# Kernel optimization log

Measured on AMD Instinct MI355X. Metric: run time of the kernel, lower is better.

The kernel has to match this reference:

```python
import jax, jax.numpy as jnp
import numpy as np

H, D, R, S, K, EV = 8, 256, 6, 2, 2, 2   # num_heads, head_dim, ratio, shared_head, topk, expand_v
HID = 2048
DV = D * EV            # head_v_dim = 512
KEY_DIM = H * D        # 2048
VAL_DIM = KEY_DIM * EV # 4096


def setup_inputs() -> dict:
    key = jax.random.key(0)
    ks = jax.random.split(key, 9)
    b, t = 2, 1024
    def lin(k, fan_in, shape):
        # ~torch default linear init scale
        return jax.random.normal(k, shape, jnp.float32) * (fan_in ** -0.5)
    return {
        "hidden_states": jax.random.normal(ks[0], (b, t, HID), jnp.float32),
        "Wq": lin(ks[1], HID, (HID, KEY_DIM)),
        "Wk": lin(ks[2], HID, (HID, KEY_DIM)),
        "Wv": lin(ks[3], HID, (HID, VAL_DIM)),
        "Wq_exp": lin(ks[4], D, (H, D, D * R)),  # per-head q expert expansion (ModuleList -> batched)
        "Wk_exp": lin(ks[5], D, (H, D, D * R)),
        "Wgate": lin(ks[6], D, (D, R - S)),
        "Wg": lin(ks[7], HID, (HID, VAL_DIM)),
        "Wo": lin(ks[8], VAL_DIM, (VAL_DIM, HID)),
    }


def reference(hidden_states, Wq, Wk, Wv, Wq_exp, Wk_exp, Wgate, Wg, Wo):
    b, t, _ = hidden_states.shape
    # base projections, split into heads: [H, b, t, D]
    q = (hidden_states @ Wq).reshape(b, t, H, D).transpose(2, 0, 1, 3)
    k = (hidden_states @ Wk).reshape(b, t, H, D).transpose(2, 0, 1, 3)
    v = (hidden_states @ Wv).reshape(b, t, H, DV)  # [b, t, H, DV]

    # --- sparse routing on q (gate over ratio - shared experts) ---
    logits = jnp.einsum('hbtd,dn->hbtn', q, Wgate)
    scores = jax.nn.softmax(logits.astype(jnp.float32), axis=-1)
    w, idx = jax.lax.top_k(scores, K)
    w = w / jnp.sum(w, axis=-1, keepdims=True)
    idx = idx + S  # shift past shared experts
    # scatter top-k weights into full [H, b, t, R]
    full = jnp.sum(jax.nn.one_hot(idx, R, dtype=w.dtype) * w[..., None], axis=-2)
    full = full.at[..., :S].set(1.0 / S)
    full = full / jnp.sum(full, axis=-1, keepdims=True)
    rw = full.astype(hidden_states.dtype).transpose(3, 1, 2, 0)  # [R, b, t, H]
    mask = (rw != 0).astype(hidden_states.dtype)                 # [R, b, t, H]

    # --- per-head expert expansions: [R, b, t, H, D] ---
    qe = jnp.einsum('hbtd,hde->hbte', q, Wq_exp).reshape(H, b, t, R, D).transpose(3, 1, 2, 0, 4)
    ke = jnp.einsum('hbtd,hde->hbte', k, Wk_exp).reshape(H, b, t, R, D).transpose(3, 1, 2, 0, 4)
    ve = jnp.broadcast_to(v[None], (R, b, t, H, DV))
    qe = qe * mask[..., None]
    ke = ke * mask[..., None]
    ve = ve * mask[..., None]

    # --- dense attention per (expert, batch, head) ---
    attn = jax.nn.softmax(jnp.einsum('rbqhd,rbkhd->rbhqk', qe, ke) / (D ** 0.5), axis=-1)
    o = jnp.einsum('rbhqk,rbkhd->rbqhd', attn, ve)  # [R, b, t, H, DV]

    # --- weighted combine over experts + gated output ---
    o = jnp.einsum('rbthd,rbth->bthd', o, rw)
    g = (hidden_states @ Wg).reshape(b, t, H, DV)
    o = o * jax.nn.silu(g)
    return o.reshape(b, t, VAL_DIM) @ Wo
```

## Files before the change

kernel.cpp:

```cpp
#include <hip/hip_runtime.h>
#include <hip/hip_bf16.h>
#include <cstdint>
#include <cstddef>

typedef __bf16 bf16_t;
typedef __bf16 bf16x8 __attribute__((ext_vector_type(8)));
typedef float f32x4 __attribute__((ext_vector_type(4)));

typedef __attribute__((address_space(3))) unsigned int lds_uint_t;
typedef __attribute__((address_space(1))) unsigned int glob_uint_t;

__device__ __forceinline__ void gload16(const void* g, void* l) {
  __builtin_amdgcn_global_load_lds((const glob_uint_t*)g, (lds_uint_t*)l, 16, 0, 0);
}

__device__ __forceinline__ f32x4 mfma16(bf16x8 a, bf16x8 b, f32x4 c) {
  return __builtin_amdgcn_mfma_f32_16x16x32_bf16(a, b, c, 0, 0, 0);
}

__global__ __launch_bounds__(256) void conv_bf16_k(const float* __restrict__ in,
                                                   bf16_t* __restrict__ out, int n8) {
  int i = blockIdx.x * 256 + threadIdx.x;
  if (i >= n8) return;
  f32x4 a = *(const f32x4*)(in + (size_t)i * 8);
  f32x4 b = *(const f32x4*)(in + (size_t)i * 8 + 4);
  bf16x8 o;
  o[0] = (bf16_t)a[0]; o[1] = (bf16_t)a[1]; o[2] = (bf16_t)a[2]; o[3] = (bf16_t)a[3];
  o[4] = (bf16_t)b[0]; o[5] = (bf16_t)b[1]; o[6] = (bf16_t)b[2]; o[7] = (bf16_t)b[3];
  *(bf16x8*)(out + (size_t)i * 8) = o;
}

__global__ __launch_bounds__(256) void tconv_k(const float* __restrict__ in, bf16_t* __restrict__ out,
                                               int R, int C, size_t inZ, size_t outZ) {
  __shared__ __align__(16) bf16_t t[64 * 72];
  in += (size_t)blockIdx.z * inZ;
  out += (size_t)blockIdx.z * outZ;
  const int c0 = blockIdx.x * 64, r0 = blockIdx.y * 64;
  const int tid = threadIdx.x;
#pragma unroll
  for (int it = 0; it < 4; it++) {
    int c = tid + it * 256;
    int row = c >> 4, ch = c & 15;
    f32x4 v = *(const f32x4*)(in + (size_t)(r0 + row) * C + c0 + ch * 4);
#pragma unroll
    for (int j = 0; j < 4; j++) t[(ch * 4 + j) * 72 + row] = (bf16_t)v[j];
  }
  __syncthreads();
#pragma unroll
  for (int it = 0; it < 2; it++) {
    int c = tid + it * 256;
    int oc = c >> 3, ch = c & 7;
    bf16x8 v = *(const bf16x8*)(t + oc * 72 + ch * 8);
    *(bf16x8*)(out + (size_t)(c0 + oc) * R + r0 + ch * 8) = v;
  }
}

__global__ __launch_bounds__(256) void tv_k(const bf16_t* __restrict__ v, bf16_t* __restrict__ Vt) {
  __shared__ __align__(16) bf16_t t[64 * 72];
  const int tt0 = blockIdx.x * 64;
  const int dv0 = blockIdx.y * 64;
  const int bh = blockIdx.z;
  const int b = bh >> 3, h = bh & 7;
  const int tid = threadIdx.x;
  const bf16_t* src = v + (size_t)(b * 1024 + tt0) * 12288 + 8192 + h * 512 + dv0;
#pragma unroll
  for (int it = 0; it < 2; it++) {
    int c = tid + it * 256;
    int row = c >> 3, ch = c & 7;
    bf16x8 x = *(const bf16x8*)(src + (size_t)row * 12288 + ch * 8);
#pragma unroll
    for (int j = 0; j < 8; j++) t[(ch * 8 + j) * 72 + row] = x[j];
  }
  __syncthreads();
  bf16_t* dst = Vt + (size_t)bh * 524288 + (size_t)dv0 * 1024 + tt0;
#pragma unroll
  for (int it = 0; it < 2; it++) {
    int c = tid + it * 256;
    int od = c >> 3, ch = c & 7;
    bf16x8 x = *(const bf16x8*)(t + od * 72 + ch * 8);
    *(bf16x8*)(dst + (size_t)od * 1024 + ch * 8) = x;
  }
}

__global__ __launch_bounds__(256) void wfuse_k(const float* __restrict__ Wq, const float* __restrict__ Wgate,
                                               float* __restrict__ Wf) {
  __shared__ float wg[1024];
  const int tid = threadIdx.x;
  for (int i = tid; i < 1024; i += 256) wg[i] = Wgate[i];
  __syncthreads();
  const int kk = blockIdx.x * 64 + (tid & 63);
  const int oid = tid >> 6;
  float acc[8] = {0, 0, 0, 0, 0, 0, 0, 0};
  const float* wr = Wq + (size_t)kk * 2048;
#pragma unroll
  for (int half = 0; half < 2; half++) {
    const int h = oid * 2 + half;
    const float* seg = wr + h * 256;
    for (int d = 0; d < 256; d += 4) {
      f32x4 q4 = *(const f32x4*)(seg + d);
#pragma unroll
      for (int n = 0; n < 4; n++) {
        acc[half * 4 + n] += q4[0] * wg[(d + 0) * 4 + n] + q4[1] * wg[(d + 1) * 4 + n] +
                             q4[2] * wg[(d + 2) * 4 + n] + q4[3] * wg[(d + 3) * 4 + n];
      }
    }
  }
#pragma unroll
  for (int jj = 0; jj < 8; jj++) Wf[(size_t)kk * 32 + oid * 8 + jj] = acc[jj];
}

__global__ __launch_bounds__(256) void logits_k(const float* __restrict__ hs, const float* __restrict__ Wf,
                                                float* __restrict__ lg) {
  __shared__ __align__(16) float hrow[2048];
  __shared__ float red[8][32];
  const int bt = blockIdx.x;
  const int tid = threadIdx.x;
  const float* src = hs + (size_t)bt * 2048;
  for (int i = tid; i < 512; i += 256) *(f32x4*)&hrow[i * 4] = *(const f32x4*)(src + i * 4);
  __syncthreads();
  const int j = tid & 31, part = tid >> 5;
  float acc = 0.f;
  for (int kk = part * 256; kk < part * 256 + 256; kk++) acc += hrow[kk] * Wf[(size_t)kk * 32 + j];
  red[part][j] = acc;
  __syncthreads();
  if (tid < 32) {
    float s = 0.f;
#pragma unroll
    for (int p = 0; p < 8; p++) s += red[p][tid];
    lg[(size_t)bt * 32 + tid] = s;
  }
}

__global__ __launch_bounds__(256) void routing_k(const float* __restrict__ lg, float* __restrict__ rw) {
  int gid = blockIdx.x * 256 + threadIdx.x;
  if (gid >= 16384) return;
  const int h = gid >> 11;
  const int bt = gid & 2047;
  const int b = bt >> 10, tt = bt & 1023;
  f32x4 l = *(const f32x4*)(lg + (size_t)bt * 32 + h * 4);
  float mx = fmaxf(fmaxf(l[0], l[1]), fmaxf(l[2], l[3]));
  float e0 = __expf(l[0] - mx), e1 = __expf(l[1] - mx), e2 = __expf(l[2] - mx), e3 = __expf(l[3] - mx);
  float den = e0 + e1 + e2 + e3;
  float s[4] = {e0 / den, e1 / den, e2 / den, e3 / den};
  int i1 = 0;
#pragma unroll
  for (int i = 1; i < 4; i++) if (s[i] > s[i1]) i1 = i;
  int i2 = (i1 == 0) ? 1 : 0;
#pragma unroll
  for (int i = 0; i < 4; i++) if (i != i1 && s[i] > s[i2]) i2 = i;
  float sw = s[i1] + s[i2];
  float w1 = s[i1] / sw, w2 = s[i2] / sw;
  float tot = 1.0f + w1 + w2;
  float o[6] = {0.5f / tot, 0.5f / tot, 0.f, 0.f, 0.f, 0.f};
  o[2 + i1] = w1 / tot;
  o[2 + i2] = w2 / tot;
#pragma unroll
  for (int r = 0; r < 6; r++) rw[(size_t)((r * 2 + b) * 8 + h) * 1024 + tt] = o[r];
}

template <int MODE>
__global__ __launch_bounds__(256) void gemm_bt(const bf16_t* __restrict__ A, const bf16_t* __restrict__ B,
                                               void* __restrict__ Cp, int K, int lda, int ldb, int ldc) {
  __shared__ __align__(16) bf16_t lsA[128 * 64];
  __shared__ __align__(16) bf16_t lsB[128 * 64];
  const int tid = threadIdx.x;
  const int lane = tid & 63, wv = tid >> 6;
  const int lrow = lane & 15, lgrp = lane >> 4;
  const int wr = wv >> 1, wc = wv & 1;
  const int bn = blockIdx.x * 128, bm = blockIdx.y * 128;

  f32x4 zero = {0.f, 0.f, 0.f, 0.f};
  f32x4 acc[4][4];
#pragma unroll
  for (int i = 0; i < 4; i++)
#pragma unroll
    for (int j = 0; j < 4; j++) acc[i][j] = zero;

  for (int k0 = 0; k0 < K; k0 += 64) {
    __syncthreads();
#pragma unroll
    for (int it = 0; it < 4; it++) {
      int c = tid + it * 256;
      int row = c >> 3, coff = (c & 7) * 16;
      gload16((const char*)A + ((size_t)(bm + row) * lda + k0) * 2 + coff, (char*)lsA + row * 128 + coff);
      gload16((const char*)B + ((size_t)(bn + row) * ldb + k0) * 2 + coff, (char*)lsB + row * 128 + coff);
    }
    __syncthreads();
#pragma unroll
    for (int kk = 0; kk < 2; kk++) {
      bf16x8 af[4], bfr[4];
#pragma unroll
      for (int m4 = 0; m4 < 4; m4++)
        af[m4] = *(const bf16x8*)((const char*)lsA + (wr * 64 + m4 * 16 + lrow) * 128 + kk * 64 + lgrp * 16);
#pragma unroll
      for (int n4 = 0; n4 < 4; n4++)
        bfr[n4] = *(const bf16x8*)((const char*)lsB + (wc * 64 + n4 * 16 + lrow) * 128 + kk * 64 + lgrp * 16);
#pragma unroll
      for (int m4 = 0; m4 < 4; m4++)
#pragma unroll
        for (int n4 = 0; n4 < 4; n4++) acc[m4][n4] = mfma16(af[m4], bfr[n4], acc[m4][n4]);
    }
  }
#pragma unroll
  for (int m4 = 0; m4 < 4; m4++) {
#pragma unroll
    for (int i = 0; i < 4; i++) {
      const int row = bm + wr * 64 + m4 * 16 + lgrp * 4 + i;
#pragma unroll
      for (int n4 = 0; n4 < 4; n4++) {
        const int col = bn + wc * 64 + n4 * 16 + lrow;
        float v = acc[m4][n4][i];
        if constexpr (MODE == 0) {
          ((bf16_t*)Cp)[(size_t)row * ldc + col] = (bf16_t)v;
        } else {
          ((float*)Cp)[(size_t)row * ldc + col] = v;
        }
      }
    }
  }
}

__global__ __launch_bounds__(256) void gemm_n64(const bf16_t* __restrict__ A, const bf16_t* __restrict__ B,
                                                float* __restrict__ C, int K, int lda, int ldb, int ldc) {
  __shared__ __align__(16) bf16_t lsA[128 * 64];
  __shared__ __align__(16) bf16_t lsB[64 * 64];
  const int tid = threadIdx.x;
  const int lane = tid & 63, wr = tid >> 6;
  const int lrow = lane & 15, lgrp = lane >> 4;
  const int bn = blockIdx.x * 64, bm = blockIdx.y * 128;

  f32x4 zero = {0.f, 0.f, 0.f, 0.f};
  f32x4 acc[2][4];
#pragma unroll
  for (int i = 0; i < 2; i++)
#pragma unroll
    for (int j = 0; j < 4; j++) acc[i][j] = zero;

  for (int k0 = 0; k0 < K; k0 += 64) {
    __syncthreads();
#pragma unroll
    for (int it = 0; it < 4; it++) {
      int c = tid + it * 256;
      int row = c >> 3, coff = (c & 7) * 16;
      gload16((const char*)A + ((size_t)(bm + row) * lda + k0) * 2 + coff, (char*)lsA + row * 128 + coff);
    }
#pragma unroll
    for (int it = 0; it < 2; it++) {
      int c = tid + it * 256;
      int row = c >> 3, coff = (c & 7) * 16;
      gload16((const char*)B + ((size_t)(bn + row) * ldb + k0) * 2 + coff, (char*)lsB + row * 128 + coff);
    }
    __syncthreads();
#pragma unroll
    for (int kk = 0; kk < 2; kk++) {
      bf16x8 af[2], bfr[4];
#pragma unroll
      for (int m2 = 0; m2 < 2; m2++)
        af[m2] = *(const bf16x8*)((const char*)lsA + (wr * 32 + m2 * 16 + lrow) * 128 + kk * 64 + lgrp * 16);
#pragma unroll
      for (int n4 = 0; n4 < 4; n4++)
        bfr[n4] = *(const bf16x8*)((const char*)lsB + (n4 * 16 + lrow) * 128 + kk * 64 + lgrp * 16);
#pragma unroll
      for (int m2 = 0; m2 < 2; m2++)
#pragma unroll
        for (int n4 = 0; n4 < 4; n4++) acc[m2][n4] = mfma16(af[m2], bfr[n4], acc[m2][n4]);
    }
  }
#pragma unroll
  for (int m2 = 0; m2 < 2; m2++) {
#pragma unroll
    for (int i = 0; i < 4; i++) {
      const int row = bm + wr * 32 + m2 * 16 + lgrp * 4 + i;
#pragma unroll
      for (int n4 = 0; n4 < 4; n4++) {
        C[(size_t)row * ldc + bn + n4 * 16 + lrow] = acc[m2][n4][i];
      }
    }
  }
}

__global__ __launch_bounds__(256) void gemm_exp(const bf16_t* __restrict__ qkg, const bf16_t* __restrict__ Wqe,
                                                const bf16_t* __restrict__ Wke, bf16_t* __restrict__ qeB,
                                                bf16_t* __restrict__ keB) {
  __shared__ __align__(16) bf16_t lsA[128 * 64];
  __shared__ __align__(16) bf16_t lsB[128 * 64];
  const int tid = threadIdx.x;
  const int lane = tid & 63, wv = tid >> 6;
  const int lrow = lane & 15, lgrp = lane >> 4;
  const int wr = wv >> 1, wc = wv & 1;
  const int bn = blockIdx.x * 128, bm = blockIdx.y * 128;
  const int z = blockIdx.z;
  const int sel = z >> 3, hh = z & 7;
  const bf16_t* A = qkg + sel * 2048 + hh * 256;
  const bf16_t* B = (sel ? Wke : Wqe) + (size_t)hh * 393216;
  bf16_t* C = sel ? keB : qeB;

  f32x4 zero = {0.f, 0.f, 0.f, 0.f};
  f32x4 acc[4][4];
#pragma unroll
  for (int i = 0; i < 4; i++)
#pragma unroll
    for (int j = 0; j < 4; j++) acc[i][j] = zero;

  for (int k0 = 0; k0 < 256; k0 += 64) {
    __syncthreads();
#pragma unroll
    for (int it = 0; it < 4; it++) {
      int c = tid + it * 256;
      int row = c >> 3, coff = (c & 7) * 16;
      gload16((const char*)A + ((size_t)(bm + row) * 12288 + k0) * 2 + coff, (char*)lsA + row * 128 + coff);
      gload16((const char*)B + ((size_t)(bn + row) * 256 + k0) * 2 + coff, (char*)lsB + row * 128 + coff);
    }
    __syncthreads();
#pragma unroll
    for (int kk = 0; kk < 2; kk++) {
      bf16x8 af[4], bfr[4];
#pragma unroll
      for (int m4 = 0; m4 < 4; m4++)
        af[m4] = *(const bf16x8*)((const char*)lsA + (wr * 64 + m4 * 16 + lrow) * 128 + kk * 64 + lgrp * 16);
#pragma unroll
      for (int n4 = 0; n4 < 4; n4++)
        bfr[n4] = *(const bf16x8*)((const char*)lsB + (wc * 64 + n4 * 16 + lrow) * 128 + kk * 64 + lgrp * 16);
#pragma unroll
      for (int m4 = 0; m4 < 4; m4++)
#pragma unroll
        for (int n4 = 0; n4 < 4; n4++) acc[m4][n4] = mfma16(af[m4], bfr[n4], acc[m4][n4]);
    }
  }
#pragma unroll
  for (int m4 = 0; m4 < 4; m4++) {
#pragma unroll
    for (int i = 0; i < 4; i++) {
      const int row = bm + wr * 64 + m4 * 16 + lgrp * 4 + i;
      const int bb = row >> 10, tt = row & 1023;
#pragma unroll
      for (int n4 = 0; n4 < 4; n4++) {
        const int col = bn + wc * 64 + n4 * 16 + lrow;
        const int rr = col >> 8, dd = col & 255;
        C[((size_t)((rr * 2 + bb) * 8 + hh) * 1024 + tt) * 256 + dd] = (bf16_t)acc[m4][n4][i];
      }
    }
  }
}

__global__ __launch_bounds__(256, 2) void attn_k(const bf16_t* __restrict__ qe, const bf16_t* __restrict__ ke,
                                                 const bf16_t* __restrict__ Vt, const float* __restrict__ rw,
                                                 const bf16_t* __restrict__ g, bf16_t* __restrict__ oc) {
  __shared__ __align__(16) bf16_t ldsK[2][32 * 256];
  __shared__ __align__(16) bf16_t ldsV[2][256 * 32];
  __shared__ __align__(16) bf16_t ldsP[4 * 16 * 40];

  const int f = (blockIdx.x & 7) * 64 + (blockIdx.x >> 3);
  const int qt = f & 15, dvh = (f >> 4) & 1, bh = f >> 5;

  const int tid = threadIdx.x;
  const int wv = tid >> 6, lane = tid & 63;
  const int lrow = lane & 15, lgrp = lane >> 4;
  const int b = bh >> 3, h = bh & 7;
  const int qw = qt * 64 + wv * 16;

  const char* vbase = (const char*)Vt + ((size_t)bh * 524288 + (size_t)dvh * 262144) * 2;

  auto issue_tile = [&](int rr, int kt, int buf) {
    const char* kb = (const char*)ke + ((size_t)((rr * 2 + b) * 8 + h) * 262144 + (size_t)kt * 8192) * 2;
    char* lk = (char*)ldsK[buf];
#pragma unroll
    for (int it = 0; it < 4; it++) {
      int p = (wv * 4 + it) * 1024 + (lane << 4);
      int row = p >> 9, off = p & 511;
      gload16(kb + (size_t)row * 512 + (off ^ ((row & 7) << 4)), lk + p);
    }
    const char* vb = vbase + kt * 64;
    char* lv = (char*)ldsV[buf];
#pragma unroll
    for (int it = 0; it < 4; it++) {
      int p = (wv * 4 + it) * 1024 + (lane << 4);
      int row = p >> 6, off = p & 63;
      gload16(vb + (size_t)row * 2048 + (off ^ (((row >> 1) & 3) << 4)), lv + p);
    }
  };

  f32x4 zero = {0.f, 0.f, 0.f, 0.f};
  f32x4 Otot[16];
#pragma unroll
  for (int n = 0; n < 16; n++) Otot[n] = zero;

  int cur = 0;
  issue_tile(0, 0, 0);

  for (int r = 0; r < 6; r++) {
    const size_t rbh = (size_t)((r * 2 + b) * 8 + h);
    const bf16_t* qbase = qe + rbh * 262144;
    const float* rwb = rw + rbh * 1024;

    bf16x8 qf[8];
#pragma unroll
    for (int c = 0; c < 8; c++)
      qf[c] = *(const bf16x8*)(qbase + (size_t)(qw + lrow) * 256 + c * 32 + lgrp * 8);
    float rwq[4];
#pragma unroll
    for (int i = 0; i < 4; i++) rwq[i] = rwb[qw + lgrp * 4 + i];

    float Lp[4] = {0.f, 0.f, 0.f, 0.f};
    f32x4 accO[16];
#pragma unroll
    for (int n = 0; n < 16; n++) accO[n] = zero;

    for (int kt = 0; kt < 32; kt++) {
      asm volatile("s_waitcnt vmcnt(0) lgkmcnt(0)" ::: "memory");
      __syncthreads();
      {
        int nr = r + ((kt == 31) ? 1 : 0);
        int nkt = (kt + 1) & 31;
        if (nr < 6) issue_tile(nr, nkt, cur ^ 1);
      }
      const char* lK = (const char*)ldsK[cur];
      const char* lV = (const char*)ldsV[cur];
      const float* rwk = rwb + kt * 32;
      float mk0 = rwk[lrow], mk1 = rwk[16 + lrow];

      f32x4 sac0 = zero, sac1 = zero;
      __builtin_amdgcn_s_setprio(1);
#pragma unroll
      for (int c = 0; c < 8; c++) {
        int col = (c * 64 + lgrp * 16) ^ ((lrow & 7) << 4);
        bf16x8 k0 = *(const bf16x8*)(lK + (size_t)lrow * 512 + col);
        bf16x8 k1 = *(const bf16x8*)(lK + (size_t)(16 + lrow) * 512 + col);
        sac0 = mfma16(qf[c], k0, sac0);
        sac1 = mfma16(qf[c], k1, sac1);
      }
      __builtin_amdgcn_s_setprio(0);
      bf16_t* pb = ldsP + wv * 640;
#pragma unroll
      for (int i = 0; i < 4; i++) {
        float e0 = __expf(sac0[i] * 0.0625f);
        float e1 = __expf(sac1[i] * 0.0625f);
        pb[(i * 4 + lgrp) * 40 + lrow] = (bf16_t)((mk0 != 0.f) ? e0 : 0.f);
        pb[(i * 4 + lgrp) * 40 + 16 + lrow] = (bf16_t)((mk1 != 0.f) ? e1 : 0.f);
        Lp[i] += ((mk0 != 0.f) ? e0 : 1.f) + ((mk1 != 0.f) ? e1 : 1.f);
      }
      bf16x8 pa = *(const bf16x8*)(pb + ((lrow & 3) * 4 + (lrow >> 2)) * 40 + lgrp * 8);
      __builtin_amdgcn_s_setprio(1);
#pragma unroll
      for (int n = 0; n < 16; n++) {
        int row = n * 16 + lrow;
        int col = (lgrp * 16) ^ (((row >> 1) & 3) << 4);
        bf16x8 vf = *(const bf16x8*)(lV + (size_t)row * 64 + col);
        accO[n] = mfma16(pa, vf, accO[n]);
      }
      __builtin_amdgcn_s_setprio(0);
      cur ^= 1;
    }
#pragma unroll
    for (int i = 0; i < 4; i++) {
      float v = Lp[i];
      v += __shfl_xor(v, 1, 16);
      v += __shfl_xor(v, 2, 16);
      v += __shfl_xor(v, 4, 16);
      v += __shfl_xor(v, 8, 16);
      float inv = rwq[i] / v;
#pragma unroll
      for (int n = 0; n < 16; n++) Otot[n][i] += accO[n][i] * inv;
    }
  }

#pragma unroll
  for (int i = 0; i < 4; i++) {
    const size_t grow = ((size_t)(b * 1024 + qw + lgrp * 4 + i)) * 12288 + 4096 + h * 512 + dvh * 256;
    const size_t orow = ((size_t)(b * 1024 + qw + lgrp * 4 + i)) * 4096 + h * 512 + dvh * 256;
#pragma unroll
    for (int n = 0; n < 16; n++) {
      float gv = (float)g[grow + n * 16 + lrow];
      float sg = gv / (1.f + __expf(-gv));
      oc[orow + n * 16 + lrow] = (bf16_t)(Otot[n][i] * sg);
    }
  }
}

extern "C" void kernel_launch(void* const* d_in, const int* in_sizes, int n_in,
                              void* d_out, int out_size, void* d_ws, size_t ws_size,
                              hipStream_t stream) {
  const float* hs  = (const float*)d_in[0];
  const float* Wq  = (const float*)d_in[1];
  const float* Wk  = (const float*)d_in[2];
  const float* Wv  = (const float*)d_in[3];
  const float* Wqe = (const float*)d_in[4];
  const float* Wke = (const float*)d_in[5];
  const float* Wgt = (const float*)d_in[6];
  const float* Wg  = (const float*)d_in[7];
  const float* Wo  = (const float*)d_in[8];
  float* out = (float*)d_out;

  const size_t MB = 1024 * 1024;
  char* w = (char*)d_ws;
  bf16_t* hs_bf = (bf16_t*)(w + 0 * MB);
  bf16_t* WcatT = (bf16_t*)(w + 8 * MB);
  bf16_t* qeB   = (bf16_t*)(w + 0 * MB);
  bf16_t* WoT   = (bf16_t*)(w + 56 * MB);
  bf16_t* WqeT  = (bf16_t*)(w + 72 * MB);
  bf16_t* WkeT  = (bf16_t*)(w + 78 * MB);
  bf16_t* qkg   = (bf16_t*)(w + 84 * MB);
  bf16_t* Vt    = (bf16_t*)(w + 132 * MB);
  bf16_t* keB   = (bf16_t*)(w + 148 * MB);
  bf16_t* ocB   = (bf16_t*)(w + 196 * MB);
  float*  Wf    = (float*)(w + 212 * MB);
  float*  lg    = (float*)(w + 212 * MB + 262144);
  float*  rwB   = (float*)(w + 212 * MB + 524288);
  (void)ws_size; (void)in_sizes; (void)n_in; (void)out_size;

  conv_bf16_k<<<2048, 256, 0, stream>>>(hs, hs_bf, 524288);
  tconv_k<<<dim3(32, 32, 1), 256, 0, stream>>>(Wq, WcatT, 2048, 2048, 0, 0);
  tconv_k<<<dim3(32, 32, 1), 256, 0, stream>>>(Wk, WcatT + 2048 * 2048, 2048, 2048, 0, 0);
  tconv_k<<<dim3(64, 32, 1), 256, 0, stream>>>(Wg, WcatT + 4096 * 2048, 2048, 4096, 0, 0);
  tconv_k<<<dim3(64, 32, 1), 256, 0, stream>>>(Wv, WcatT + 8192 * 2048, 2048, 4096, 0, 0);
  tconv_k<<<dim3(32, 64, 1), 256, 0, stream>>>(Wo, WoT, 4096, 2048, 0, 0);
  tconv_k<<<dim3(24, 4, 8), 256, 0, stream>>>(Wqe, WqeT, 256, 1536, 393216, 393216);
  tconv_k<<<dim3(24, 4, 8), 256, 0, stream>>>(Wke, WkeT, 256, 1536, 393216, 393216);

  wfuse_k<<<32, 256, 0, stream>>>(Wq, Wgt, Wf);
  logits_k<<<2048, 256, 0, stream>>>(hs, Wf, lg);
  routing_k<<<64, 256, 0, stream>>>(lg, rwB);

  gemm_bt<0><<<dim3(96, 16, 1), 256, 0, stream>>>(hs_bf, WcatT, qkg, 2048, 2048, 2048, 12288);
  tv_k<<<dim3(16, 8, 16), 256, 0, stream>>>(qkg, Vt);

  gemm_exp<<<dim3(12, 16, 16), 256, 0, stream>>>(qkg, WqeT, WkeT, qeB, keB);

  attn_k<<<512, 256, 0, stream>>>(qeB, keB, Vt, rwB, qkg, ocB);

  gemm_n64<<<dim3(32, 16, 1), 256, 0, stream>>>(ocB, WoT, out, 4096, 4096, 4096, 2048);
}
```

Measured before the change: 701.0 us.

## Compact active keys per routed expert and skip masked key tiles in attention

Adds an index-compaction kernel that lists, for each routed expert and (batch, head), the key positions where the routing weight is nonzero. A gather kernel builds a compacted transposed V for those positions. The attention loop for routed experts then walks only the active key tiles, gathering K rows through indices held in LDS. Masked keys are accounted for analytically through the softmax denominator init. This cuts the QK and PV work for routed experts to roughly the active fraction, at the cost of extra kernels, an indirect K load, and losing cross-expert prefetch of the first tile.

Result: no change. 701.0 us (-0.0%).

```diff
diff --git a/kernel.cpp b/kernel.cpp
--- a/kernel.cpp
+++ b/kernel.cpp
@@ -158,6 +158,73 @@
   for (int r = 0; r < 6; r++) rw[(size_t)((r * 2 + b) * 8 + h) * 1024 + tt] = o[r];
 }
 
+__global__ __launch_bounds__(256) void idx_k(const float* __restrict__ rw, int* __restrict__ kidx,
+                                             float* __restrict__ maskg, int2* __restrict__ kn) {
+  __shared__ int wsum[4];
+  const int z = blockIdx.x;
+  const int rr = z >> 4, bh = z & 15;
+  const int b = bh >> 3, h = bh & 7;
+  const float* rwp = rw + (size_t)(((rr + 2) * 2 + b) * 8 + h) * 1024;
+  const int tid = threadIdx.x;
+  const int lane = tid & 63, wv = tid >> 6;
+  int act[4];
+  int c = 0;
+#pragma unroll
+  for (int j = 0; j < 4; j++) { act[j] = (rwp[tid * 4 + j] != 0.f) ? 1 : 0; c += act[j]; }
+  int s = c;
+  for (int o = 1; o < 64; o <<= 1) { int t = __shfl_up(s, o, 64); if (lane >= o) s += t; }
+  if (lane == 63) wsum[wv] = s;
+  __syncthreads();
+  int base = 0;
+  for (int wi = 0; wi < wv; wi++) base += wsum[wi];
+  int excl = base + s - c;
+  int Na = wsum[0] + wsum[1] + wsum[2] + wsum[3];
+  int* kout = kidx + (size_t)z * 1088;
+  float* mout = maskg + (size_t)z * 1088;
+  int o = excl;
+#pragma unroll
+  for (int j = 0; j < 4; j++)
+    if (act[j]) { kout[o] = tid * 4 + j; mout[o] = 1.f; o++; }
+  for (int i = Na + tid; i < 1088; i += 256) { kout[i] = 0; mout[i] = 0.f; }
+  if (tid == 0) kn[z] = make_int2(Na, (Na + 63) & ~63);
+}
+
+__global__ __launch_bounds__(256) void vgather_k(const bf16_t* __restrict__ qkg, const int* __restrict__ kidx,
+                                                 const int2* __restrict__ kn, bf16_t* __restrict__ Vg) {
+  __shared__ __align__(16) bf16_t t[64 * 72];
+  __shared__ int idx[64];
+  const int z = blockIdx.z;
+  const int rr = z >> 4, bh = z & 15;
+  const int b = bh >> 3, h = bh & 7;
+  int2 k = kn[z];
+  const int s0 = blockIdx.x * 64;
+  if (s0 >= k.y) return;
+  const int dv0 = blockIdx.y * 64;
+  const int tid = threadIdx.x;
+  if (tid < 64) idx[tid] = kidx[(size_t)z * 1088 + s0 + tid];
+  __syncthreads();
+  int base = 0;
+  for (int r2 = 0; r2 < rr; r2++) base += kn[r2 * 16 + bh].y;
+#pragma unroll
+  for (int it = 0; it < 2; it++) {
+    int cc = tid + it * 256;
+    int row = cc >> 3, ch = cc & 7;
+    const bf16_t* src = qkg + (size_t)(b * 1024 + idx[row]) * 12288 + 8192 + h * 512 + dv0 + ch * 8;
+    bf16x8 x = *(const bf16x8*)src;
+#pragma unroll
+    for (int j = 0; j < 8; j++) t[(ch * 8 + j) * 72 + row] = x[j];
+  }
+  __syncthreads();
+  bf16_t* dst = Vg + (size_t)(bh * 512 + dv0) * 2304 + base + s0;
+#pragma unroll
+  for (int it = 0; it < 2; it++) {
+    int cc = tid + it * 256;
+    int od = cc >> 3, ch = cc & 7;
+    bf16x8 x = *(const bf16x8*)(t + od * 72 + ch * 8);
+    *(bf16x8*)(dst + (size_t)od * 2304 + ch * 8) = x;
+  }
+}
+
 template <int MODE>
 __global__ __launch_bounds__(256) void gemm_bt(const bf16_t* __restrict__ A, const bf16_t* __restrict__ B,
                                                void* __restrict__ Cp, int K, int lda, int ldb, int ldc) {
@@ -345,10 +412,13 @@
 
 __global__ __launch_bounds__(256, 2) void attn_k(const bf16_t* __restrict__ qe, const bf16_t* __restrict__ ke,
                                                  const bf16_t* __restrict__ Vt, const float* __restrict__ rw,
-                                                 const bf16_t* __restrict__ g, bf16_t* __restrict__ oc) {
+                                                 const bf16_t* __restrict__ g, bf16_t* __restrict__ oc,
+                                                 const int* __restrict__ kidx, const float* __restrict__ maskg,
+                                                 const int2* __restrict__ kn, const bf16_t* __restrict__ Vg) {
   __shared__ __align__(16) bf16_t ldsK[2][32 * 256];
   __shared__ __align__(16) bf16_t ldsV[2][256 * 32];
   __shared__ __align__(16) bf16_t ldsP[4 * 16 * 40];
+  __shared__ int ldsIdx[1088];
 
   const int f = (blockIdx.x & 7) * 64 + (blockIdx.x >> 3);
   const int qt = f & 15, dvh = (f >> 4) & 1, bh = f >> 5;
@@ -359,26 +429,7 @@
   const int b = bh >> 3, h = bh & 7;
   const int qw = qt * 64 + wv * 16;
 
-  const char* vbase = (const char*)Vt + ((size_t)bh * 524288 + (size_t)dvh * 262144) * 2;
-
-  auto issue_tile = [&](int rr, int kt, int buf) {
-    const char* kb = (const char*)ke + ((size_t)((rr * 2 + b) * 8 + h) * 262144 + (size_t)kt * 8192) * 2;
-    char* lk = (char*)ldsK[buf];
-#pragma unroll
-    for (int it = 0; it < 4; it++) {
-      int p = (wv * 4 + it) * 1024 + (lane << 4);
-      int row = p >> 9, off = p & 511;
-      gload16(kb + (size_t)row * 512 + (off ^ ((row & 7) << 4)), lk + p);
-    }
-    const char* vb = vbase + kt * 64;
-    char* lv = (char*)ldsV[buf];
-#pragma unroll
-    for (int it = 0; it < 4; it++) {
-      int p = (wv * 4 + it) * 1024 + (lane << 4);
-      int row = p >> 6, off = p & 63;
-      gload16(vb + (size_t)row * 2048 + (off ^ (((row >> 1) & 3) << 4)), lv + p);
-    }
-  };
+  const char* vtb = (const char*)Vt + ((size_t)bh * 524288 + (size_t)dvh * 262144) * 2;
 
   f32x4 zero = {0.f, 0.f, 0.f, 0.f};
   f32x4 Otot[16];
@@ -386,12 +437,34 @@
   for (int n = 0; n < 16; n++) Otot[n] = zero;
 
   int cur = 0;
-  issue_tile(0, 0, 0);
-
   for (int r = 0; r < 6; r++) {
     const size_t rbh = (size_t)((r * 2 + b) * 8 + h);
     const bf16_t* qbase = qe + rbh * 262144;
     const float* rwb = rw + rbh * 1024;
+    const char* kbr = (const char*)ke + rbh * 524288;
+
+    int nkt = 32;
+    float lpinit = 0.f;
+    const float* mgp = nullptr;
+    const char* vgb = vtb;
+    size_t vstride = 2048;
+    const bool routed = (r >= 2);
+    if (routed) {
+      const int rr = r - 2;
+      int2 kkn = kn[rr * 16 + bh];
+      nkt = kkn.y >> 5;
+      lpinit = (float)(1024 - kkn.x) * 0.0625f;
+      int basep = 0;
+      for (int r2 = 0; r2 < rr; r2++) basep += kn[r2 * 16 + bh].y;
+      vgb = (const char*)Vg + ((size_t)(bh * 512 + dvh * 256) * 2304 + basep) * 2;
+      vstride = 4608;
+      mgp = maskg + (size_t)(rr * 16 + bh) * 1088;
+      __syncthreads();
+      const int* kp = kidx + (size_t)(rr * 16 + bh) * 1088;
+      for (int i = tid; i < 1088; i += 256) ldsIdx[i] = kp[i];
+      __syncthreads();
+    }
+    if (nkt == 0) continue;
 
     bf16x8 qf[8];
 #pragma unroll
@@ -401,23 +474,48 @@
 #pragma unroll
     for (int i = 0; i < 4; i++) rwq[i] = rwb[qw + lgrp * 4 + i];
 
-    float Lp[4] = {0.f, 0.f, 0.f, 0.f};
+    float Lp[4] = {lpinit, lpinit, lpinit, lpinit};
     f32x4 accO[16];
 #pragma unroll
     for (int n = 0; n < 16; n++) accO[n] = zero;
 
-    for (int kt = 0; kt < 32; kt++) {
+    auto issue_tile = [&](int kt, int buf) {
+      char* lk = (char*)ldsK[buf];
+      if (!routed) {
+#pragma unroll
+        for (int it = 0; it < 4; it++) {
+          int p = (wv * 4 + it) * 1024 + (lane << 4);
+          int row = p >> 9, off = p & 511;
+          gload16(kbr + (size_t)(kt * 32 + row) * 512 + (off ^ ((row & 7) << 4)), lk + p);
+        }
+      } else {
+#pragma unroll
+        for (int it = 0; it < 4; it++) {
+          int p = (wv * 4 + it) * 1024 + (lane << 4);
+          int row = p >> 9, off = p & 511;
+          int iv = ldsIdx[kt * 32 + row];
+          gload16(kbr + (size_t)iv * 512 + (off ^ ((row & 7) << 4)), lk + p);
+        }
+      }
+      char* lv = (char*)ldsV[buf];
+      const char* vb = vgb + (size_t)kt * 64;
+#pragma unroll
+      for (int it = 0; it < 4; it++) {
+        int p = (wv * 4 + it) * 1024 + (lane << 4);
+        int row = p >> 6, off = p & 63;
+        gload16(vb + (size_t)row * vstride + (off ^ (((row >> 1) & 3) << 4)), lv + p);
+      }
+    };
+
+    issue_tile(0, cur);
+    for (int kt = 0; kt < nkt; kt++) {
       asm volatile("s_waitcnt vmcnt(0) lgkmcnt(0)" ::: "memory");
       __syncthreads();
-      {
-        int nr = r + ((kt == 31) ? 1 : 0);
-        int nkt = (kt + 1) & 31;
-        if (nr < 6) issue_tile(nr, nkt, cur ^ 1);
-      }
+      if (kt + 1 < nkt) issue_tile(kt + 1, cur ^ 1);
       const char* lK = (const char*)ldsK[cur];
       const char* lV = (const char*)ldsV[cur];
-      const float* rwk = rwb + kt * 32;
-      float mk0 = rwk[lrow], mk1 = rwk[16 + lrow];
+      float mg0 = 1.f, mg1 = 1.f;
+      if (routed) { mg0 = mgp[kt * 32 + lrow]; mg1 = mgp[kt * 32 + 16 + lrow]; }
 
       f32x4 sac0 = zero, sac1 = zero;
       __builtin_amdgcn_s_setprio(1);
@@ -433,11 +531,11 @@
       bf16_t* pb = ldsP + wv * 640;
 #pragma unroll
       for (int i = 0; i < 4; i++) {
-        float e0 = __expf(sac0[i] * 0.0625f);
-        float e1 = __expf(sac1[i] * 0.0625f);
-        pb[(i * 4 + lgrp) * 40 + lrow] = (bf16_t)((mk0 != 0.f) ? e0 : 0.f);
-        pb[(i * 4 + lgrp) * 40 + 16 + lrow] = (bf16_t)((mk1 != 0.f) ? e1 : 0.f);
-        Lp[i] += ((mk0 != 0.f) ? e0 : 1.f) + ((mk1 != 0.f) ? e1 : 1.f);
+        float p0 = mg0 * __expf(sac0[i] * 0.0625f);
+        float p1 = mg1 * __expf(sac1[i] * 0.0625f);
+        pb[(i * 4 + lgrp) * 40 + lrow] = (bf16_t)p0;
+        pb[(i * 4 + lgrp) * 40 + 16 + lrow] = (bf16_t)p1;
+        Lp[i] += p0 + p1;
       }
       bf16x8 pa = *(const bf16x8*)(pb + ((lrow & 3) * 4 + (lrow >> 2)) * 40 + lgrp * 8);
       __builtin_amdgcn_s_setprio(1);
@@ -506,6 +604,10 @@
   float*  Wf    = (float*)(w + 212 * MB);
   float*  lg    = (float*)(w + 212 * MB + 262144);
   float*  rwB   = (float*)(w + 212 * MB + 524288);
+  bf16_t* VgB   = (bf16_t*)(w + 214 * MB);
+  int*    kidxB = (int*)(w + 250 * MB);
+  float*  maskgB= (float*)(w + 250 * MB + 524288);
+  int2*   knB   = (int2*)(w + 250 * MB + 1048576);
   (void)ws_size; (void)in_sizes; (void)n_in; (void)out_size;
 
   conv_bf16_k<<<2048, 256, 0, stream>>>(hs, hs_bf, 524288);
@@ -520,13 +622,15 @@
   wfuse_k<<<32, 256, 0, stream>>>(Wq, Wgt, Wf);
   logits_k<<<2048, 256, 0, stream>>>(hs, Wf, lg);
   routing_k<<<64, 256, 0, stream>>>(lg, rwB);
+  idx_k<<<64, 256, 0, stream>>>(rwB, kidxB, maskgB, knB);
 
   gemm_bt<0><<<dim3(96, 16, 1), 256, 0, stream>>>(hs_bf, WcatT, qkg, 2048, 2048, 2048, 12288);
   tv_k<<<dim3(16, 8, 16), 256, 0, stream>>>(qkg, Vt);
+  vgather_k<<<dim3(16, 8, 64), 256, 0, stream>>>(qkg, kidxB, knB, VgB);
 
   gemm_exp<<<dim3(12, 16, 16), 256, 0, stream>>>(qkg, WqeT, WkeT, qeB, keB);
 
-  attn_k<<<512, 256, 0, stream>>>(qeB, keB, Vt, rwB, qkg, ocB);
+  attn_k<<<512, 256, 0, stream>>>(qeB, keB, Vt, rwB, qkg, ocB, kidxB, maskgB, knB, VgB);
 
   gemm_n64<<<dim3(32, 16, 1), 256, 0, stream>>>(ocB, WoT, out, 4096, 4096, 4096, 2048);
 }
```
